# Kernel optimization log

Measured on AMD Instinct MI355X. Metric: run time of the kernel, lower is better.

The kernel has to match this reference:

```python
import jax, jax.numpy as jnp
import numpy as np

DIM, H, WH, WW = 192, 6, 8, 8
N = WH * WW
B = 4096
NW = 64
HALF = DIM // 2
HD = DIM // H


def _make_buffers():
    # continuous relative coords table (1, 2WH-1, 2WW-1, 2), Swin-V2 style
    rh = np.arange(-(WH - 1), WH, dtype=np.float32)
    rw = np.arange(-(WW - 1), WW, dtype=np.float32)
    gh, gw = np.meshgrid(rh, rw, indexing='ij')
    tab = np.stack([gh, gw], axis=-1)[None]  # (1, 2WH-1, 2WW-1, 2)
    tab[..., 0] /= WH - 1
    tab[..., 1] /= WW - 1
    tab *= 3.2
    tab = np.sign(tab) * (1.0 - np.exp(-np.abs(tab)))
    # relative position index (N, N) int
    ch, cw = np.meshgrid(np.arange(WH), np.arange(WW), indexing='ij')
    coords = np.stack([ch, cw]).reshape(2, -1)  # (2, N)
    rel = coords[:, :, None] - coords[:, None, :]  # (2, N, N)
    rel = rel.transpose(1, 2, 0).astype(np.int64)
    rel[:, :, 0] += WH - 1
    rel[:, :, 1] += WW - 1
    rel[:, :, 0] *= 2 * WW - 1
    idx = rel.sum(-1)  # (N, N)
    return jnp.asarray(tab, jnp.float32), jnp.asarray(idx, jnp.int32)


def setup_inputs() -> dict:
    key = jax.random.key(0)
    ks = jax.random.split(key, 24)
    w = lambda k, shape: jax.random.normal(k, shape, jnp.float32) * 0.02
    rpb_table, rp_index = _make_buffers()
    inp = {
        'x': jax.random.normal(ks[0], (B, N, DIM), jnp.float32),
        'mask': jnp.zeros((NW, N, N), jnp.float32),
        'logit_scale': jnp.log(10.0) * jnp.ones((H, 1, 1), jnp.float32),
        'mlp_w1': w(ks[1], (128, 2)), 'mlp_b1': jnp.zeros((128,), jnp.float32),
        'mlp_w2': w(ks[2], (H, 128)),
        'q1w': w(ks[3], (HALF, HALF)), 'q1b': jnp.zeros((HALF,), jnp.float32),
        'q2w': w(ks[4], (HALF, HALF)), 'q2b': jnp.zeros((HALF,), jnp.float32),
        'k1w': w(ks[5], (HALF, HALF)), 'k1b': jnp.zeros((HALF,), jnp.float32),
        'k2w': w(ks[6], (HALF, HALF)), 'k2b': jnp.zeros((HALF,), jnp.float32),
        'v1w': w(ks[7], (HALF, HALF)), 'v1b': jnp.zeros((HALF,), jnp.float32),
        'v2w': w(ks[8], (HALF, HALF)), 'v2b': jnp.zeros((HALF,), jnp.float32),
        'p1w': w(ks[9], (HALF, HALF)), 'p1b': jnp.zeros((HALF,), jnp.float32),
        'p2w': w(ks[10], (HALF, HALF)), 'p2b': jnp.zeros((HALF,), jnp.float32),
        'rpb_table': rpb_table,
        'rp_index': rp_index,
    }
    return inp


def _lin(x, w, b):
    return x @ w.T + b


def _l2n(x):
    return x / jnp.maximum(jnp.linalg.norm(x, axis=-1, keepdims=True), 1e-12)


def reference(x, mask, logit_scale, mlp_w1, mlp_b1, mlp_w2,
              q1w, q1b, q2w, q2b, k1w, k1b, k2w, k2b, v1w, v1b, v2w, v2b,
              p1w, p1b, p2w, p2b, rpb_table, rp_index):
    b, n, c = x.shape
    h, hd = H, c // H
    x0, x1 = x[..., :c // 2], x[..., c // 2:]
    # split-channel GRL residual projections, then concat halves -> heads
    def heads(y0w, y0b, y1w, y1b):
        y = jnp.concatenate([x0 + _lin(x0, y0w, y0b), x1 + _lin(x1, y1w, y1b)], -1)
        return y.reshape(b, n, h, hd).transpose(0, 2, 1, 3)  # (b, h, n, hd)
    q = heads(q1w, q1b, q2w, q2b)
    k = heads(k1w, k1b, k2w, k2b)
    v = heads(v1w, v1b, v2w, v2b)
    # cosine attention with learned per-head logit scale
    attn = jnp.einsum('bhnd,bhmd->bhnm', _l2n(q), _l2n(k))
    scale = jnp.exp(jnp.minimum(logit_scale, jnp.log(jnp.float32(100.0))))  # (h,1,1)
    attn = attn * scale
    # ESRPB: MLP over continuous relative coords -> per-head bias
    tab = jax.nn.relu(rpb_table @ mlp_w1.T + mlp_b1) @ mlp_w2.T  # (1, 2WH-1, 2WW-1, h)
    tab = tab.reshape(-1, h)
    rpb = tab[rp_index.reshape(-1)].reshape(n, n, h).transpose(2, 0, 1)  # (h, n, n)
    attn = attn + 16.0 * jax.nn.sigmoid(rpb)[None]
    nw = mask.shape[0]
    attn = (attn.reshape(b // nw, nw, h, n, n) + mask[None, :, None]).reshape(b, h, n, n)
    attn = jax.nn.softmax(attn, axis=-1)
    out = jnp.einsum('bhnm,bhmd->bhnd', attn, v).transpose(0, 2, 1, 3).reshape(b, n, c)
    o0, o1 = out[..., :c // 2], out[..., c // 2:]
    return jnp.concatenate([_lin(o0, p1w, p1b), _lin(o1, p2w, p2b)], -1)
```

## Files before the change

### kernel.cpp

```cpp
#include <hip/hip_runtime.h>
#include <hip/hip_bf16.h>

#define NT 64
#define DM 192
#define LOG2E 1.4426950408889634f

typedef __attribute__((ext_vector_type(4))) float f32x4;
typedef __attribute__((ext_vector_type(4))) float float4v;
using half2v = __attribute__((ext_vector_type(2))) _Float16;
using half4v = __attribute__((ext_vector_type(4))) _Float16;
using half8v = __attribute__((ext_vector_type(8))) _Float16;

#define BIAS_OFF  147456
#define TAB_OFF   6438912
#define SCALE_OFF 6444312

__device__ __forceinline__ half4v pk4(float a, float b, float c, float d){
  half2v lo = __builtin_bit_cast(half2v, __builtin_amdgcn_cvt_pkrtz(a, b));
  half2v hi = __builtin_bit_cast(half2v, __builtin_amdgcn_cvt_pkrtz(c, d));
  half4v r; r[0]=lo[0]; r[1]=lo[1]; r[2]=hi[0]; r[3]=hi[1];
  return r;
}
__device__ __forceinline__ float exp2v(float x){
  float r;
  asm("v_exp_f32 %0, %1" : "=v"(r) : "v"(x));
  return r;
}

__global__ __launch_bounds__(384) void pre_a(
  const float* __restrict__ q1w, const float* __restrict__ q2w,
  const float* __restrict__ k1w, const float* __restrict__ k2w,
  const float* __restrict__ v1w, const float* __restrict__ v2w,
  const float* __restrict__ p1w, const float* __restrict__ p2w,
  const float* __restrict__ w1, const float* __restrict__ b1,
  const float* __restrict__ w2, const float* __restrict__ rpbt,
  const float* __restrict__ ls, char* __restrict__ ws)
{
  int blk = blockIdx.x, t = threadIdx.x;
  if (blk < 48) {
    const float* Ws[8] = {q1w,q2w,k1w,k2w,v1w,v2w,p1w,p2w};
    int mat = blk / 6, ct = blk % 6;
    int lane = t & 63, ks = t >> 6;
    if (ks < 3) {
      const float* W = Ws[mat];
      int c  = 16*ct + (lane & 15);
      int d0 = 32*ks + 8*(lane >> 4);
      half8v h;
      #pragma unroll
      for (int j = 0; j < 8; ++j) {
        float wel = W[c*96 + d0 + j];
        if (mat < 6 && c == d0 + j) wel += 1.0f;
        h[j] = (_Float16)wel;
      }
      *(half8v*)(ws + (size_t)((mat*6+ct)*3+ks)*1024 + lane*16) = h;
    }
  } else {
    float* tab = (float*)(ws + TAB_OFF);
    if (t < 225) {
      float t0 = rpbt[2*t], t1 = rpbt[2*t+1];
      float acc[6] = {0,0,0,0,0,0};
      for (int j = 0; j < 128; ++j) {
        float hv = fmaxf(t0*w1[2*j] + t1*w1[2*j+1] + b1[j], 0.f);
        #pragma unroll
        for (int hh = 0; hh < 6; ++hh) acc[hh] += hv * w2[hh*128 + j];
      }
      #pragma unroll
      for (int hh = 0; hh < 6; ++hh) tab[t*6 + hh] = acc[hh];
    }
    if (t >= 240 && t < 246) {
      float* sc = (float*)(ws + SCALE_OFF);
      int i = t - 240;
      sc[i] = expf(fminf(ls[i], 4.605170185988091f)) * LOG2E;
    }
  }
}

__global__ __launch_bounds__(256) void pre_b(
  const float* __restrict__ mask, const int* __restrict__ rpi,
  char* __restrict__ ws)
{
  int w = blockIdx.x / 6, h = blockIdx.x % 6;
  int lane = threadIdx.x & 63, nt = threadIdx.x >> 6;
  const float* tab = (const float*)(ws + TAB_OFF);
  float* bias = (float*)(ws + BIAS_OFF);
  #pragma unroll
  for (int mt = 0; mt < 4; ++mt)
    #pragma unroll
    for (int r = 0; r < 4; ++r) {
      int m = 16*mt + ((lane >> 4) << 2) + r;
      int n = 16*nt + (lane & 15);
      int idx = rpi[n*64 + m];
      float tv = tab[idx*6 + h];
      float sg = 16.f / (1.f + expf(-tv));
      float mv = mask[(w*64 + n)*64 + m];
      bias[(size_t)(((w*6+h)*4+mt)*4+nt)*256 + lane*4 + r] = (sg + mv) * LOG2E;
    }
}

__global__ __launch_bounds__(768, 2) void win_attn(
  const float* __restrict__ x, const char* __restrict__ ws,
  const float* __restrict__ q1b, const float* __restrict__ q2b,
  const float* __restrict__ k1b, const float* __restrict__ k2b,
  const float* __restrict__ v1b, const float* __restrict__ v2b,
  const float* __restrict__ p1b, const float* __restrict__ p2b,
  float* __restrict__ out)
{
  __shared__ __align__(16) _Float16 xo2[2][64*200];
  const int tid = threadIdx.x;
  const int wv = tid >> 6, lane = tid & 63;
  const int llo = lane & 15, lhi = lane >> 4;
  const int wgrp = (wv >= 6) ? 1 : 0;
  const int h = wv - 6*wgrp;
  const int b = blockIdx.x*2 + wgrp, w_in = b & 63;
  const int lt = tid - 384*wgrp;
  _Float16* xo = xo2[wgrp];
  const int half = (h < 3) ? 0 : 1;
  const int hd0 = 32 * (h % 3);
  const f32x4 zf = {0.f,0.f,0.f,0.f};
  const float* xg = x + (size_t)b * (NT*DM);

  float4v xv[8];
  #pragma unroll
  for (int it = 0; it < 8; ++it) xv[it] = *(const float4v*)(xg + 4*(lt + it*384));
  #pragma unroll
  for (int it = 0; it < 8; ++it) {
    int f4 = lt + it*384;
    int row = f4 / 48, c4 = f4 % 48;
    *(half4v*)(xo + row*200 + c4*4) = pk4(xv[it][0], xv[it][1], xv[it][2], xv[it][3]);
  }
  __syncthreads();

  const float scale_h = ((const float*)(ws + SCALE_OFF))[h];

  half4v qf[2][4], kf[2][4];
  {
    const float* qbp = half ? q2b : q1b;
    const float* kbp = half ? k2b : k1b;
    f32x4 qacc[2][4], kacc[2][4];
    #pragma unroll
    for (int dt = 0; dt < 2; ++dt) {
      f32x4 qb = *(const f32x4*)(qbp + hd0 + 16*dt + 4*lhi);
      f32x4 kb = *(const f32x4*)(kbp + hd0 + 16*dt + 4*lhi);
      #pragma unroll
      for (int tt = 0; tt < 4; ++tt) { qacc[dt][tt] = qb; kacc[dt][tt] = kb; }
    }
    __builtin_amdgcn_s_setprio(1);
    #pragma unroll
    for (int ks = 0; ks < 3; ++ks) {
      half8v xf[4];
      #pragma unroll
      for (int tt = 0; tt < 4; ++tt)
        xf[tt] = *(const half8v*)(xo + (16*tt+llo)*200 + half*96 + 32*ks + 8*lhi);
      #pragma unroll
      for (int dt = 0; dt < 2; ++dt) {
        half8v wq = *(const half8v*)(ws + (size_t)(((0+half)*6 + 2*(h%3)+dt)*3 + ks)*1024 + lane*16);
        half8v wk = *(const half8v*)(ws + (size_t)(((2+half)*6 + 2*(h%3)+dt)*3 + ks)*1024 + lane*16);
        #pragma unroll
        for (int tt = 0; tt < 4; ++tt) {
          qacc[dt][tt] = __builtin_amdgcn_mfma_f32_16x16x32_f16(wq, xf[tt], qacc[dt][tt], 0,0,0);
          kacc[dt][tt] = __builtin_amdgcn_mfma_f32_16x16x32_f16(wk, xf[tt], kacc[dt][tt], 0,0,0);
        }
      }
    }
    __builtin_amdgcn_s_setprio(0);
    #pragma unroll
    for (int tt = 0; tt < 4; ++tt) {
      float sq = 0.f, sk = 0.f;
      #pragma unroll
      for (int dt = 0; dt < 2; ++dt)
        #pragma unroll
        for (int r = 0; r < 4; ++r) {
          sq += qacc[dt][tt][r]*qacc[dt][tt][r];
          sk += kacc[dt][tt][r]*kacc[dt][tt][r];
        }
      sq += __shfl_xor(sq, 16); sq += __shfl_xor(sq, 32);
      sk += __shfl_xor(sk, 16); sk += __shfl_xor(sk, 32);
      float invq = scale_h / fmaxf(sqrtf(sq), 1e-12f);
      float invk = 1.f / fmaxf(sqrtf(sk), 1e-12f);
      #pragma unroll
      for (int dt = 0; dt < 2; ++dt) {
        qf[dt][tt] = pk4(qacc[dt][tt][0]*invq, qacc[dt][tt][1]*invq,
                         qacc[dt][tt][2]*invq, qacc[dt][tt][3]*invq);
        kf[dt][tt] = pk4(kacc[dt][tt][0]*invk, kacc[dt][tt][1]*invk,
                         kacc[dt][tt][2]*invk, kacc[dt][tt][3]*invk);
      }
    }
  }

  const float4v* biasf = (const float4v*)(ws + BIAS_OFF);
  half4v pf[4][4];
  float inv_s[4];
  #pragma unroll
  for (int nt = 0; nt < 4; ++nt) {
    f32x4 s[4];
    #pragma unroll
    for (int mt = 0; mt < 4; ++mt) {
      f32x4 bb = *(const f32x4*)&biasf[(size_t)(((w_in*6 + h)*4 + mt)*4 + nt)*64 + lane];
      f32x4 t0 = __builtin_amdgcn_mfma_f32_16x16x16f16(kf[0][mt], qf[0][nt], bb, 0,0,0);
      s[mt]    = __builtin_amdgcn_mfma_f32_16x16x16f16(kf[1][mt], qf[1][nt], t0, 0,0,0);
    }
    float mx = s[0][0];
    #pragma unroll
    for (int mt = 0; mt < 4; ++mt)
      #pragma unroll
      for (int r = 0; r < 4; ++r) mx = fmaxf(mx, s[mt][r]);
    mx = fmaxf(mx, __shfl_xor(mx, 16)); mx = fmaxf(mx, __shfl_xor(mx, 32));
    float e[4][4]; float sum = 0.f;
    #pragma unroll
    for (int mt = 0; mt < 4; ++mt)
      #pragma unroll
      for (int r = 0; r < 4; ++r) { e[mt][r] = exp2v(s[mt][r] - mx); sum += e[mt][r]; }
    sum += __shfl_xor(sum, 16); sum += __shfl_xor(sum, 32);
    inv_s[nt] = 1.f / sum;
    #pragma unroll
    for (int mt = 0; mt < 4; ++mt)
      pf[mt][nt] = pk4(e[mt][0], e[mt][1], e[mt][2], e[mt][3]);
  }

  half4v vf[4][2];
  {
    const float* vbp = half ? v2b : v1b;
    f32x4 acc[4][2];
    #pragma unroll
    for (int ct = 0; ct < 2; ++ct) {
      float vb = vbp[hd0 + 16*ct + llo];
      f32x4 vbv = {vb, vb, vb, vb};
      #pragma unroll
      for (int tt = 0; tt < 4; ++tt) acc[tt][ct] = vbv;
    }
    #pragma unroll
    for (int ks = 0; ks < 3; ++ks) {
      half8v xf[4];
      #pragma unroll
      for (int tt = 0; tt < 4; ++tt)
        xf[tt] = *(const half8v*)(xo + (16*tt+llo)*200 + half*96 + 32*ks + 8*lhi);
      #pragma unroll
      for (int ct = 0; ct < 2; ++ct) {
        half8v wvf = *(const half8v*)(ws + (size_t)(((4+half)*6 + 2*(h%3)+ct)*3 + ks)*1024 + lane*16);
        #pragma unroll
        for (int tt = 0; tt < 4; ++tt)
          acc[tt][ct] = __builtin_amdgcn_mfma_f32_16x16x32_f16(xf[tt], wvf, acc[tt][ct], 0,0,0);
      }
    }
    #pragma unroll
    for (int ct = 0; ct < 2; ++ct)
      #pragma unroll
      for (int tt = 0; tt < 4; ++tt)
        vf[tt][ct] = pk4(acc[tt][ct][0], acc[tt][ct][1], acc[tt][ct][2], acc[tt][ct][3]);
  }

  f32x4 oacc[2][4];
  #pragma unroll
  for (int dt = 0; dt < 2; ++dt)
    #pragma unroll
    for (int nt = 0; nt < 4; ++nt) oacc[dt][nt] = zf;
  __builtin_amdgcn_s_setprio(1);
  #pragma unroll
  for (int mt = 0; mt < 4; ++mt)
    #pragma unroll
    for (int dt = 0; dt < 2; ++dt)
      #pragma unroll
      for (int nt = 0; nt < 4; ++nt)
        oacc[dt][nt] = __builtin_amdgcn_mfma_f32_16x16x16f16(vf[mt][dt], pf[mt][nt], oacc[dt][nt], 0,0,0);
  __builtin_amdgcn_s_setprio(0);

  __syncthreads();
  #pragma unroll
  for (int dt = 0; dt < 2; ++dt)
    #pragma unroll
    for (int nt = 0; nt < 4; ++nt)
      *(half4v*)(xo + (16*nt+llo)*200 + 32*h + 16*dt + 4*lhi) =
        pk4(oacc[dt][nt][0]*inv_s[nt], oacc[dt][nt][1]*inv_s[nt],
            oacc[dt][nt][2]*inv_s[nt], oacc[dt][nt][3]*inv_s[nt]);
  __syncthreads();

  const int ph = h & 1;
  const int cp = h >> 1;
  const float* pbp = ph ? p2b : p1b;
  f32x4 facc[2][4];
  #pragma unroll
  for (int cc = 0; cc < 2; ++cc) {
    f32x4 pb = *(const f32x4*)(pbp + 16*(2*cp+cc) + 4*lhi);
    #pragma unroll
    for (int nt = 0; nt < 4; ++nt) facc[cc][nt] = pb;
  }
  #pragma unroll
  for (int ks = 0; ks < 3; ++ks) {
    half8v of[4];
    #pragma unroll
    for (int nt = 0; nt < 4; ++nt)
      of[nt] = *(const half8v*)(xo + (16*nt+llo)*200 + 96*ph + 32*ks + 8*lhi);
    #pragma unroll
    for (int cc = 0; cc < 2; ++cc) {
      half8v wp = *(const half8v*)(ws + (size_t)(((6+ph)*6 + 2*cp+cc)*3 + ks)*1024 + lane*16);
      #pragma unroll
      for (int nt = 0; nt < 4; ++nt)
        facc[cc][nt] = __builtin_amdgcn_mfma_f32_16x16x32_f16(wp, of[nt], facc[cc][nt], 0,0,0);
    }
  }
  float* og = out + (size_t)b * (NT*DM);
  #pragma unroll
  for (int cc = 0; cc < 2; ++cc)
    #pragma unroll
    for (int nt = 0; nt < 4; ++nt) {
      float4v res = {facc[cc][nt][0], facc[cc][nt][1], facc[cc][nt][2], facc[cc][nt][3]};
      *(float4v*)(og + (size_t)(16*nt+llo)*192 + 96*ph + 16*(2*cp+cc) + 4*lhi) = res;
    }
}

extern "C" void kernel_launch(void* const* d_in, const int* in_sizes, int n_in,
                              void* d_out, int out_size, void* d_ws, size_t ws_size,
                              hipStream_t stream)
{
  const float* x    = (const float*)d_in[0];
  const float* mask = (const float*)d_in[1];
  const float* ls   = (const float*)d_in[2];
  const float* w1   = (const float*)d_in[3];
  const float* b1   = (const float*)d_in[4];
  const float* w2   = (const float*)d_in[5];
  const float* q1w  = (const float*)d_in[6];  const float* q1b = (const float*)d_in[7];
  const float* q2w  = (const float*)d_in[8];  const float* q2b = (const float*)d_in[9];
  const float* k1w  = (const float*)d_in[10]; const float* k1b = (const float*)d_in[11];
  const float* k2w  = (const float*)d_in[12]; const float* k2b = (const float*)d_in[13];
  const float* v1w  = (const float*)d_in[14]; const float* v1b = (const float*)d_in[15];
  const float* v2w  = (const float*)d_in[16]; const float* v2b = (const float*)d_in[17];
  const float* p1w  = (const float*)d_in[18]; const float* p1b = (const float*)d_in[19];
  const float* p2w  = (const float*)d_in[20]; const float* p2b = (const float*)d_in[21];
  const float* rpbt = (const float*)d_in[22];
  const int*   rpi  = (const int*)d_in[23];
  char* ws = (char*)d_ws;
  float* o = (float*)d_out;

  pre_a<<<49, 384, 0, stream>>>(q1w,q2w,k1w,k2w,v1w,v2w,p1w,p2w, w1,b1,w2, rpbt, ls, ws);
  pre_b<<<384, 256, 0, stream>>>(mask, rpi, ws);
  win_attn<<<2048, 768, 0, stream>>>(x, ws, q1b,q2b,k1b,k2b,v1b,v2b,p1b,p2b, o);
}
```

Baseline: 202.8 us.

## Remap block order, use fast rsq/rcp, tree reductions, and MFMA priority hints

Remaps blockIdx so that consecutive blocks process windows in a strided order, aiming to change cache locality for x and the bias table across CUs/XCDs. It replaces sqrt+divide normalization with hardware rsq and the softmax reciprocal with rcp, and rewrites the max/sum reductions as balanced trees to shorten dependency chains. It also adds s_setprio raises around the QK and V MFMA loops. The fast intrinsics slightly change numerics, and the remapping assumes the grid size is a multiple of 512 blocks.

```diff
diff --git a/kernel.cpp b/kernel.cpp
--- a/kernel.cpp
+++ b/kernel.cpp
@@ -111,7 +111,11 @@
   const int llo = lane & 15, lhi = lane >> 4;
   const int wgrp = (wv >= 6) ? 1 : 0;
   const int h = wv - 6*wgrp;
-  const int b = blockIdx.x*2 + wgrp, w_in = b & 63;
+  const int B = blockIdx.x;
+  const int g = (((B >> 3) >> 6) << 3) | (B & 7);
+  const int kk = (B >> 3) & 63;
+  const int b0 = kk*32 + g;
+  const int b = b0*2 + wgrp, w_in = b & 63;
   const int lt = tid - 384*wgrp;
   _Float16* xo = xo2[wgrp];
   const int half = (h < 3) ? 0 : 1;
@@ -165,25 +169,20 @@
     __builtin_amdgcn_s_setprio(0);
     #pragma unroll
     for (int tt = 0; tt < 4; ++tt) {
-      float sq = 0.f, sk = 0.f;
-      #pragma unroll
-      for (int dt = 0; dt < 2; ++dt)
-        #pragma unroll
-        for (int r = 0; r < 4; ++r) {
-          sq += qacc[dt][tt][r]*qacc[dt][tt][r];
-          sk += kacc[dt][tt][r]*kacc[dt][tt][r];
-        }
+      f32x4 q0 = qacc[0][tt], q1 = qacc[1][tt];
+      f32x4 k0 = kacc[0][tt], k1 = kacc[1][tt];
+      float sq = ((q0[0]*q0[0] + q0[1]*q0[1]) + (q0[2]*q0[2] + q0[3]*q0[3]))
+               + ((q1[0]*q1[0] + q1[1]*q1[1]) + (q1[2]*q1[2] + q1[3]*q1[3]));
+      float sk = ((k0[0]*k0[0] + k0[1]*k0[1]) + (k0[2]*k0[2] + k0[3]*k0[3]))
+               + ((k1[0]*k1[0] + k1[1]*k1[1]) + (k1[2]*k1[2] + k1[3]*k1[3]));
       sq += __shfl_xor(sq, 16); sq += __shfl_xor(sq, 32);
       sk += __shfl_xor(sk, 16); sk += __shfl_xor(sk, 32);
-      float invq = scale_h / fmaxf(sqrtf(sq), 1e-12f);
-      float invk = 1.f / fmaxf(sqrtf(sk), 1e-12f);
-      #pragma unroll
-      for (int dt = 0; dt < 2; ++dt) {
-        qf[dt][tt] = pk4(qacc[dt][tt][0]*invq, qacc[dt][tt][1]*invq,
-                         qacc[dt][tt][2]*invq, qacc[dt][tt][3]*invq);
-        kf[dt][tt] = pk4(kacc[dt][tt][0]*invk, kacc[dt][tt][1]*invk,
-                         kacc[dt][tt][2]*invk, kacc[dt][tt][3]*invk);
-      }
+      float invq = scale_h * __builtin_amdgcn_rsqf(fmaxf(sq, 1e-24f));
+      float invk = __builtin_amdgcn_rsqf(fmaxf(sk, 1e-24f));
+      qf[0][tt] = pk4(q0[0]*invq, q0[1]*invq, q0[2]*invq, q0[3]*invq);
+      qf[1][tt] = pk4(q1[0]*invq, q1[1]*invq, q1[2]*invq, q1[3]*invq);
+      kf[0][tt] = pk4(k0[0]*invk, k0[1]*invk, k0[2]*invk, k0[3]*invk);
+      kf[1][tt] = pk4(k1[0]*invk, k1[1]*invk, k1[2]*invk, k1[3]*invk);
     }
   }
 
@@ -193,25 +192,32 @@
   #pragma unroll
   for (int nt = 0; nt < 4; ++nt) {
     f32x4 s[4];
+    __builtin_amdgcn_s_setprio(1);
     #pragma unroll
     for (int mt = 0; mt < 4; ++mt) {
       f32x4 bb = *(const f32x4*)&biasf[(size_t)(((w_in*6 + h)*4 + mt)*4 + nt)*64 + lane];
       f32x4 t0 = __builtin_amdgcn_mfma_f32_16x16x16f16(kf[0][mt], qf[0][nt], bb, 0,0,0);
       s[mt]    = __builtin_amdgcn_mfma_f32_16x16x16f16(kf[1][mt], qf[1][nt], t0, 0,0,0);
     }
-    float mx = s[0][0];
+    __builtin_amdgcn_s_setprio(0);
+    float m0 = fmaxf(fmaxf(s[0][0], s[0][1]), fmaxf(s[0][2], s[0][3]));
+    float m1 = fmaxf(fmaxf(s[1][0], s[1][1]), fmaxf(s[1][2], s[1][3]));
+    float m2 = fmaxf(fmaxf(s[2][0], s[2][1]), fmaxf(s[2][2], s[2][3]));
+    float m3 = fmaxf(fmaxf(s[3][0], s[3][1]), fmaxf(s[3][2], s[3][3]));
+    float mx = fmaxf(fmaxf(m0, m1), fmaxf(m2, m3));
+    mx = fmaxf(mx, __shfl_xor(mx, 16)); mx = fmaxf(mx, __shfl_xor(mx, 32));
+    float e[4][4];
     #pragma unroll
     for (int mt = 0; mt < 4; ++mt)
       #pragma unroll
-      for (int r = 0; r < 4; ++r) mx = fmaxf(mx, s[mt][r]);
-    mx = fmaxf(mx, __shfl_xor(mx, 16)); mx = fmaxf(mx, __shfl_xor(mx, 32));
-    float e[4][4]; float sum = 0.f;
-    #pragma unroll
-    for (int mt = 0; mt < 4; ++mt)
-      #pragma unroll
-      for (int r = 0; r < 4; ++r) { e[mt][r] = exp2v(s[mt][r] - mx); sum += e[mt][r]; }
+      for (int r = 0; r < 4; ++r) e[mt][r] = exp2v(s[mt][r] - mx);
+    float t0s = (e[0][0]+e[0][1]) + (e[0][2]+e[0][3]);
+    float t1s = (e[1][0]+e[1][1]) + (e[1][2]+e[1][3]);
+    float t2s = (e[2][0]+e[2][1]) + (e[2][2]+e[2][3]);
+    float t3s = (e[3][0]+e[3][1]) + (e[3][2]+e[3][3]);
+    float sum = (t0s+t1s) + (t2s+t3s);
     sum += __shfl_xor(sum, 16); sum += __shfl_xor(sum, 32);
-    inv_s[nt] = 1.f / sum;
+    inv_s[nt] = __builtin_amdgcn_rcpf(sum);
     #pragma unroll
     for (int mt = 0; mt < 4; ++mt)
       pf[mt][nt] = pk4(e[mt][0], e[mt][1], e[mt][2], e[mt][3]);
@@ -228,6 +234,7 @@
       #pragma unroll
       for (int tt = 0; tt < 4; ++tt) acc[tt][ct] = vbv;
     }
+    __builtin_amdgcn_s_setprio(1);
     #pragma unroll
     for (int ks = 0; ks < 3; ++ks) {
       half8v xf[4];
@@ -242,6 +249,7 @@
           acc[tt][ct] = __builtin_amdgcn_mfma_f32_16x16x32_f16(xf[tt], wvf, acc[tt][ct], 0,0,0);
       }
     }
+    __builtin_amdgcn_s_setprio(0);
     #pragma unroll
     for (int ct = 0; ct < 2; ++ct)
       #pragma unroll
```

Measured after the change: 197.4 us. 2.6% less time.
